# Performance work log

Hardware: AMD Instinct MI355X
Metric: run time of the kernel (lower is better)

The kernel has to match this reference:

```python
import jax, jax.numpy as jnp
import numpy as np

RES = 1024
DEPTH = 2.0

def setup_inputs() -> dict:
    key = jax.random.key(0)
    k1, k2 = jax.random.split(key)
    point_cloud = jax.random.normal(k1, (32, 200000, 3), dtype=jnp.float32)
    transformation_matrices = jax.random.normal(k2, (32, 3, 4), dtype=jnp.float32)
    return {"point_cloud": point_cloud, "transformation_matrices": transformation_matrices}

def reference(point_cloud, transformation_matrices):
    B, N, _ = point_cloud.shape
    R = RES
    # homogeneous transform: (B,N,4) @ (B,4,3) -> (B,N,3)
    ones = jnp.ones((B, N, 1), dtype=point_cloud.dtype)
    pc_h = jnp.concatenate([point_cloud, ones], axis=2)
    transformed = jnp.einsum('bnk,bck->bnc', pc_h, transformation_matrices)  # (B,N,3)
    normalized = transformed / DEPTH
    # pixel coords, clamped to [0, R-1]; torch int() truncates (== floor for >=0)
    px = jnp.clip((normalized[:, :, 0] + 1.0) / 2.0 * R, 0.0, R - 1)
    py = jnp.clip((1.0 - normalized[:, :, 1]) / 2.0 * R, 0.0, R - 1)
    xi = jnp.floor(px).astype(jnp.int32)
    yi = jnp.floor(py).astype(jnp.int32)
    z = normalized[:, :, 2]
    b_ids = jnp.arange(B, dtype=jnp.int32)[:, None]
    flat_pix = (b_ids * (R * R) + yi * R + xi).reshape(-1)           # (B*N,)
    gidx = jnp.arange(B * N, dtype=jnp.int32)                        # global point index; within a batch row, larger gidx == larger j
    winners = jax.ops.segment_max(gidx, flat_pix, num_segments=B * R * R)
    valid = winners >= 0                                             # empty segments get int32 min
    safe_w = jnp.clip(winners, 0)
    depth_flat = jnp.where(valid, z.reshape(-1)[safe_w], 0.0)
    depth_map = depth_flat.reshape(B, R, R)
    # F.interpolate to the same (R,R) size with bilinear/align_corners=False is the identity map.
    return depth_map
```

## Files before the change

### kernel.cpp

```cpp
#include <hip/hip_runtime.h>

#define RES   1024
#define NPTS  200000
#define NB    32
#define PPT   8
#define BLK   512
#define NBLK  49
#define BPB   4096
#define NBAND 256
#define BANDH 4
#define BORD  4096

#define OFF_AR 0
#define OFF_TM 51380224
#define OFF_BW 52985856

__global__ __launch_bounds__(256) void k_init(int4* __restrict__ bwin4)
{
    int i = blockIdx.x * 256 + threadIdx.x;
    bwin4[i] = make_int4(-1, -1, -1, -1);
}

__global__ __launch_bounds__(BLK) void k_bin(
        const float* __restrict__ pc,
        const float* __restrict__ tm,
        unsigned long long* __restrict__ arena,
        unsigned int* __restrict__ tmeta,
        int* __restrict__ bwin)
{
#pragma clang fp contract(off)
    const int b   = blockIdx.y;
    const int tid = threadIdx.x;
    const int gg  = b * NBLK + blockIdx.x;

    __shared__ int sb[BORD];
    __shared__ unsigned long long stage[BPB];
    __shared__ unsigned int hist[NBAND];
    __shared__ unsigned int lofs[NBAND];
    for (int k = tid; k < BORD; k += BLK) sb[k] = -1;
    if (tid < NBAND) hist[tid] = 0u;
    __syncthreads();

    const float* M = tm + b * 12;
    const float m0 = M[0], m1 = M[1], m2  = M[2],  m3  = M[3];
    const float m4 = M[4], m5 = M[5], m6  = M[6],  m7  = M[7];
    const float m8 = M[8], m9 = M[9], m10 = M[10], m11 = M[11];

    unsigned long long ent[PPT];
    unsigned int rb[PPT];
    const int base = blockIdx.x * BPB + tid;

    #pragma unroll
    for (int k = 0; k < PPT; ++k) {
        rb[k] = 0xFFFFFFFFu;
        int n = base + k * BLK;
        if (n < NPTS) {
            const float* p = pc + ((size_t)b * NPTS + n) * 3;
            float x = p[0], y = p[1], z = p[2];
            float tx = (x * m0 + y * m1) + (z * m2  + m3);
            float ty = (x * m4 + y * m5) + (z * m6  + m7);
            float tz = (x * m8 + y * m9) + (z * m10 + m11);
            float nx = tx * 0.5f;
            float ny = ty * 0.5f;
            float nz = tz * 0.5f;
            float px = (nx + 1.0f) * 512.0f;
            float py = (1.0f - ny) * 512.0f;
            px = fminf(fmaxf(px, 0.0f), 1023.0f);
            py = fminf(fmaxf(py, 0.0f), 1023.0f);
            int xi = (int)floorf(px);
            int yi = (int)floorf(py);

            bool border = (xi == 0) | (xi == 1023) | (yi == 0) | (yi == 1023);
            if (border) {
                int idx = (yi == 0)    ? xi
                        : (yi == 1023) ? 1024 + xi
                        : (xi == 0)    ? 2048 + yi
                                       : 3072 + yi;
                atomicMax(&sb[idx], n);
            } else {
                int bin = yi >> 2;
                unsigned r = atomicAdd(&hist[bin], 1u);
                rb[k] = ((unsigned)bin << 12) | r;
                unsigned pix = (unsigned)((yi & 3) * RES + xi);
                ent[k] = ((unsigned long long)pix << 52)
                       | ((unsigned long long)(unsigned)n << 32)
                       | (unsigned long long)__float_as_uint(nz);
            }
        }
    }
    __syncthreads();

    if (tid < 64) {
        unsigned carry = 0;
        #pragma unroll
        for (int c = 0; c < 4; ++c) {
            unsigned v = hist[c * 64 + tid];
            unsigned s = v;
            #pragma unroll
            for (int d = 1; d < 64; d <<= 1) {
                unsigned o = __shfl_up(s, d);
                if (tid >= d) s += o;
            }
            lofs[c * 64 + tid] = (s - v) + carry;
            carry += __shfl(s, 63);
        }
    }
    __syncthreads();

    if (tid < NBAND)
        tmeta[((size_t)(b * NBAND + tid)) * NBLK + blockIdx.x]
            = (lofs[tid] << 16) | hist[tid];

    #pragma unroll
    for (int k = 0; k < PPT; ++k) {
        if (rb[k] != 0xFFFFFFFFu) {
            unsigned bin = rb[k] >> 12, r = rb[k] & 4095u;
            stage[lofs[bin] + r] = ent[k];
        }
    }
    __syncthreads();

    const unsigned Ttot = lofs[NBAND - 1] + hist[NBAND - 1];
    for (unsigned k = tid; k < Ttot; k += BLK)
        arena[(size_t)gg * BPB + k] = stage[k];

    for (int k = tid; k < BORD; k += BLK) {
        int v = sb[k];
        if (v >= 0) atomicMax(&bwin[b * BORD + k], v);
    }
}

__global__ __launch_bounds__(512) void k_tile(
        const unsigned long long* __restrict__ arena,
        const unsigned int* __restrict__ tmeta,
        const int* __restrict__ bwin,
        const float* __restrict__ pc,
        const float* __restrict__ tm,
        float* __restrict__ out)
{
#pragma clang fp contract(off)
    const int bucket = blockIdx.x;
    const int b = bucket >> 8, band = bucket & 255;
    const int tid = threadIdx.x;

    __shared__ __align__(16) unsigned long long tile[BANDH * RES];
    __shared__ unsigned int pref[NBLK + 1];
    __shared__ unsigned int sbase[NBLK];

    for (int k = tid; k < BANDH * RES; k += 512) tile[k] = 0ull;

    unsigned mv = 0;
    if (tid < NBLK)
        mv = tmeta[((size_t)(b * NBAND + band)) * NBLK + tid];
    if (tid < 64) {
        unsigned cnt = (tid < NBLK) ? (mv & 0xFFFFu) : 0u;
        unsigned s = cnt;
        #pragma unroll
        for (int d = 1; d < 64; d <<= 1) {
            unsigned o = __shfl_up(s, d);
            if (tid >= d) s += o;
        }
        if (tid < NBLK) {
            pref[tid + 1] = s;
            sbase[tid] = (unsigned)((b * NBLK + tid) * BPB) + (mv >> 16);
        }
        if (tid == 0) pref[0] = 0u;
    }
    __syncthreads();

    const unsigned T = pref[NBLK];
    for (unsigned idx = tid; idx < T; idx += 512) {
        int lo = 0, hi = NBLK - 1;
        #pragma unroll
        for (int it = 0; it < 6; ++it) {
            int mid = (lo + hi + 1) >> 1;
            if (pref[mid] <= idx) lo = mid; else hi = mid - 1;
        }
        unsigned long long e = arena[(size_t)sbase[lo] + (idx - pref[lo])];
        atomicMax(&tile[e >> 52], e & 0x000FFFFFFFFFFFFFull);
    }
    __syncthreads();

    const float* M2 = tm + b * 12 + 8;
    const float m8 = M2[0], m9 = M2[1], m10 = M2[2], m11 = M2[3];
    const int y0 = band * BANDH;
    const int* bw = bwin + b * BORD;

    for (int r = 0; r < BANDH; ++r) {
        int yi = y0 + r;
        ulonglong2 kk = ((const ulonglong2*)(tile + r * RES))[tid];
        float2 o2;
        o2.x = __uint_as_float((unsigned)(kk.x & 0xFFFFFFFFull));
        o2.y = __uint_as_float((unsigned)(kk.y & 0xFFFFFFFFull));

        #pragma unroll
        for (int h = 0; h < 2; ++h) {
            int xi = tid * 2 + h;
            bool isb = (yi == 0) | (yi == 1023) | (xi == 0) | (xi == 1023);
            if (isb) {
                int n = (yi == 0)    ? bw[xi]
                      : (yi == 1023) ? bw[1024 + xi]
                      : (xi == 0)    ? bw[2048 + yi]
                                     : bw[3072 + yi];
                float zv = 0.0f;
                if (n >= 0) {
                    const float* p = pc + ((size_t)b * NPTS + n) * 3;
                    float t = (p[0] * m8 + p[1] * m9) + (p[2] * m10 + m11);
                    zv = t * 0.5f;
                }
                if (h) o2.y = zv; else o2.x = zv;
            }
        }
        ((float2*)(out + ((size_t)b * RES + yi) * RES))[tid] = o2;
    }
}

extern "C" void kernel_launch(void* const* d_in, const int* in_sizes, int n_in,
                              void* d_out, int out_size, void* d_ws, size_t ws_size,
                              hipStream_t stream)
{
    const float* pc = (const float*)d_in[0];
    const float* tm = (const float*)d_in[1];
    float* out = (float*)d_out;

    char* ws = (char*)d_ws;
    unsigned long long* arena = (unsigned long long*)(ws + OFF_AR);
    unsigned int* tmeta = (unsigned int*)(ws + OFF_TM);
    int*          bwin  = (int*)         (ws + OFF_BW);

    k_init<<<(NB * BORD / 4) / 256, 256, 0, stream>>>((int4*)bwin);

    dim3 g1(NBLK, NB);
    k_bin<<<g1, BLK, 0, stream>>>(pc, tm, arena, tmeta, bwin);

    k_tile<<<NB * NBAND, 512, 0, stream>>>(arena, tmeta, bwin, pc, tm, out);
}
```

Before: 84.85 us.

## Fold border-pixel winners into binned arena entries and drop separate border pass

Each bin block now turns its per-block border-pixel winners into regular packed arena entries (pixel, index, depth) and stages them with the interior points. The separate init kernel, the global atomicMax border buffer and the per-pixel border fixup in the tile kernel all go away. The tile kernel's output loop becomes a plain coalesced copy of the low 32 bits of the tile. This removes one launch, the global atomics and the scattered point-cloud reloads for border pixels. In exchange the bin kernel does some extra shared atomics and gathers for border points.

```diff
diff --git a/kernel.cpp b/kernel.cpp
--- a/kernel.cpp
+++ b/kernel.cpp
@@ -10,23 +10,16 @@
 #define NBAND 256
 #define BANDH 4
 #define BORD  4096
+#define SPT   (BORD/BLK)
 
 #define OFF_AR 0
 #define OFF_TM 51380224
-#define OFF_BW 52985856
-
-__global__ __launch_bounds__(256) void k_init(int4* __restrict__ bwin4)
-{
-    int i = blockIdx.x * 256 + threadIdx.x;
-    bwin4[i] = make_int4(-1, -1, -1, -1);
-}
 
 __global__ __launch_bounds__(BLK) void k_bin(
         const float* __restrict__ pc,
         const float* __restrict__ tm,
         unsigned long long* __restrict__ arena,
-        unsigned int* __restrict__ tmeta,
-        int* __restrict__ bwin)
+        unsigned int* __restrict__ tmeta)
 {
 #pragma clang fp contract(off)
     const int b   = blockIdx.y;
@@ -90,6 +83,33 @@
     }
     __syncthreads();
 
+    unsigned long long ent2[SPT];
+    unsigned int rb2[SPT];
+    #pragma unroll
+    for (int j = 0; j < SPT; ++j) {
+        rb2[j] = 0xFFFFFFFFu;
+        int k = j * BLK + tid;
+        int v = sb[k];
+        if (v >= 0) {
+            int xi, yi;
+            if      (k < 1024) { xi = k;        yi = 0;        }
+            else if (k < 2048) { xi = k - 1024; yi = 1023;     }
+            else if (k < 3072) { xi = 0;        yi = k - 2048; }
+            else               { xi = 1023;     yi = k - 3072; }
+            const float* p = pc + ((size_t)b * NPTS + v) * 3;
+            float tz = (p[0] * m8 + p[1] * m9) + (p[2] * m10 + m11);
+            float nz = tz * 0.5f;
+            int bin = yi >> 2;
+            unsigned r = atomicAdd(&hist[bin], 1u);
+            rb2[j] = ((unsigned)bin << 12) | r;
+            unsigned pix = (unsigned)((yi & 3) * RES + xi);
+            ent2[j] = ((unsigned long long)pix << 52)
+                    | ((unsigned long long)(unsigned)v << 32)
+                    | (unsigned long long)__float_as_uint(nz);
+        }
+    }
+    __syncthreads();
+
     if (tid < 64) {
         unsigned carry = 0;
         #pragma unroll
@@ -118,27 +138,25 @@
             stage[lofs[bin] + r] = ent[k];
         }
     }
+    #pragma unroll
+    for (int j = 0; j < SPT; ++j) {
+        if (rb2[j] != 0xFFFFFFFFu) {
+            unsigned bin = rb2[j] >> 12, r = rb2[j] & 4095u;
+            stage[lofs[bin] + r] = ent2[j];
+        }
+    }
     __syncthreads();
 
     const unsigned Ttot = lofs[NBAND - 1] + hist[NBAND - 1];
     for (unsigned k = tid; k < Ttot; k += BLK)
         arena[(size_t)gg * BPB + k] = stage[k];
-
-    for (int k = tid; k < BORD; k += BLK) {
-        int v = sb[k];
-        if (v >= 0) atomicMax(&bwin[b * BORD + k], v);
-    }
 }
 
 __global__ __launch_bounds__(512) void k_tile(
         const unsigned long long* __restrict__ arena,
         const unsigned int* __restrict__ tmeta,
-        const int* __restrict__ bwin,
-        const float* __restrict__ pc,
-        const float* __restrict__ tm,
         float* __restrict__ out)
 {
-#pragma clang fp contract(off)
     const int bucket = blockIdx.x;
     const int b = bucket >> 8, band = bucket & 255;
     const int tid = threadIdx.x;
@@ -181,37 +199,12 @@
     }
     __syncthreads();
 
-    const float* M2 = tm + b * 12 + 8;
-    const float m8 = M2[0], m9 = M2[1], m10 = M2[2], m11 = M2[3];
-    const int y0 = band * BANDH;
-    const int* bw = bwin + b * BORD;
-
-    for (int r = 0; r < BANDH; ++r) {
-        int yi = y0 + r;
-        ulonglong2 kk = ((const ulonglong2*)(tile + r * RES))[tid];
-        float2 o2;
-        o2.x = __uint_as_float((unsigned)(kk.x & 0xFFFFFFFFull));
-        o2.y = __uint_as_float((unsigned)(kk.y & 0xFFFFFFFFull));
-
-        #pragma unroll
-        for (int h = 0; h < 2; ++h) {
-            int xi = tid * 2 + h;
-            bool isb = (yi == 0) | (yi == 1023) | (xi == 0) | (xi == 1023);
-            if (isb) {
-                int n = (yi == 0)    ? bw[xi]
-                      : (yi == 1023) ? bw[1024 + xi]
-                      : (xi == 0)    ? bw[2048 + yi]
-                                     : bw[3072 + yi];
-                float zv = 0.0f;
-                if (n >= 0) {
-                    const float* p = pc + ((size_t)b * NPTS + n) * 3;
-                    float t = (p[0] * m8 + p[1] * m9) + (p[2] * m10 + m11);
-                    zv = t * 0.5f;
-                }
-                if (h) o2.y = zv; else o2.x = zv;
-            }
-        }
-        ((float2*)(out + ((size_t)b * RES + yi) * RES))[tid] = o2;
+    float* ob = out + (size_t)bucket * (BANDH * RES);
+    #pragma unroll
+    for (int j = 0; j < 8; ++j) {
+        int p = j * 512 + tid;
+        unsigned zbits = (unsigned)(tile[p] & 0xFFFFFFFFull);
+        ob[p] = __uint_as_float(zbits);
     }
 }
 
@@ -226,12 +219,9 @@
     char* ws = (char*)d_ws;
     unsigned long long* arena = (unsigned long long*)(ws + OFF_AR);
     unsigned int* tmeta = (unsigned int*)(ws + OFF_TM);
-    int*          bwin  = (int*)         (ws + OFF_BW);
-
-    k_init<<<(NB * BORD / 4) / 256, 256, 0, stream>>>((int4*)bwin);
 
     dim3 g1(NBLK, NB);
-    k_bin<<<g1, BLK, 0, stream>>>(pc, tm, arena, tmeta, bwin);
-
-    k_tile<<<NB * NBAND, 512, 0, stream>>>(arena, tmeta, bwin, pc, tm, out);
+    k_bin<<<g1, BLK, 0, stream>>>(pc, tm, arena, tmeta);
+
+    k_tile<<<NB * NBAND, 512, 0, stream>>>(arena, tmeta, out);
 }
```

Measured after the change: 105.7 us. +24.6%, slower.
